# Performance work log

Hardware: AMD Instinct MI355X
Metric: run time of the kernel (lower is better)

The kernel has to match this reference:

```python
import jax, jax.numpy as jnp
import numpy as np

# dims
B, N, FN, FE, H, OUT, MP = 128, 64, 64, 16, 128, 32, 4
P_EDGE = 0.125  # avg degree ~8


def _build_graph_indices():
    """Replicates the torch index construction (nonzero / per-row cat loops)
    with vectorized numpy; done once at setup since adjacency is an input."""
    rng = np.random.default_rng(0)
    up = np.triu(rng.random((B, N, N)) < P_EDGE, 1)
    A = (up | up.transpose(0, 2, 1)).astype(np.int64)  # symmetric, no self-loops
    b_idx, n_idx, nhb_idx = np.nonzero(A)              # row-major, like torch nonzero
    E = b_idx.shape[0]
    ids = np.zeros_like(A)
    ids[b_idx, n_idx, nhb_idx] = np.arange(E) + 1      # adj_of_edge_batch_indices
    deg = A.sum(-1)                                    # [B,N]
    edge_deg = deg[b_idx, nhb_idx]                     # in-degree of each edge's neighbour
    rows = ids[b_idx, nhb_idx, :]                      # [E,N]
    eb = rows[rows > 0] - 1                            # ingoing edge ids, per-row order
    igeb = np.repeat(np.arange(E), edge_deg)           # receiving edge id
    keep = n_idx[igeb] != nhb_idx[eb]                  # drop the reverse edge
    eb, igeb = eb[keep], igeb[keep]
    node_mask = deg != 0                               # [B,N]
    return A, b_idx, n_idx, nhb_idx, eb, igeb, node_mask


def setup_inputs() -> dict:
    key = jax.random.key(0)
    ks = jax.random.split(key, 9)
    A, b_idx, n_idx, nhb_idx, eb, igeb, node_mask = _build_graph_indices()
    s = lambda k, *sh: jax.random.normal(k, sh, jnp.float32) * 0.05
    return {
        "nodes": jax.random.normal(ks[0], (B, N, FN), jnp.float32),
        "edges": jax.random.normal(ks[1], (B, N, N, FE), jnp.float32),
        "W_emb": s(ks[2], FN + FN + FE, H),
        "b_emb": jnp.zeros((H,), jnp.float32),
        "W_msg": s(ks[3], H, H),
        "W_edge": s(ks[4], H, H),
        "b_prop": jnp.zeros((H,), jnp.float32),
        "W_out": s(ks[5], H, OUT),
        "b_out": jnp.zeros((OUT,), jnp.float32),
        "edges_b_idx": jnp.asarray(b_idx),
        "edges_n_idx": jnp.asarray(n_idx),
        "edges_nhb_idx": jnp.asarray(nhb_idx),
        "ing_eb_idx": jnp.asarray(eb),
        "ing_igeb_idx": jnp.asarray(igeb),
        "node_mask": jnp.asarray(node_mask),
    }


def reference(nodes, edges, W_emb, b_emb, W_msg, W_edge, b_prop, W_out, b_out,
              edges_b_idx, edges_n_idx, edges_nhb_idx, ing_eb_idx, ing_igeb_idx,
              node_mask):
    E = edges_b_idx.shape[0]
    Bn, Nn = nodes.shape[0], nodes.shape[1]
    # preprocess_edges: tanh(Linear([node; neighbour; edge]))
    cat = jnp.concatenate([
        nodes[edges_b_idx, edges_n_idx],      # [E,FN]
        nodes[edges_b_idx, edges_nhb_idx],    # [E,FN]
        edges[edges_b_idx, edges_n_idx, edges_nhb_idx],  # [E,FE]
    ], axis=-1)
    e_feat = jnp.tanh(cat @ W_emb + b_emb)    # [E,H]
    # edge-memory message passing; scatter(set)+masked sum == segment_sum over
    # the filtered ingoing-edge pairs (unset slots are zero in the original)
    mem = jnp.zeros((E, W_emb.shape[1]), cat.dtype)
    for _ in range(MP):
        msg = jax.ops.segment_sum(mem[ing_eb_idx], ing_igeb_idx, num_segments=E)
        mem = jnp.tanh(msg @ W_msg + e_feat @ W_edge + b_prop)
    # node_sets scatter + sum over degree slots == segment_sum per receiving node
    node_seg = edges_b_idx * Nn + edges_n_idx
    graph_sets = jax.ops.segment_sum(mem, node_seg, num_segments=Bn * Nn)
    graph_sets = graph_sets.reshape(Bn, Nn, -1)   # [B,N,H]
    # readout: masked sum over nodes, then linear
    g = (graph_sets * node_mask[..., None].astype(cat.dtype)).sum(1)  # [B,H]
    return g @ W_out + b_out
```

## Files before the change

kernel.cpp:

```cpp
#include <hip/hip_runtime.h>
#include <hip/hip_bf16.h>

#define NB 128
#define NN 64
#define HH 128

typedef short bf16x8 __attribute__((ext_vector_type(8)));
typedef float f32x4 __attribute__((ext_vector_type(4)));

static inline int cdiv(int a, int b) { return (a + b - 1) / b; }

__device__ __forceinline__ float tanh_fast(float x) {
    float ax = fabsf(x);
    float ex = __expf(-2.0f * ax);
    float t  = (1.0f - ex) / (1.0f + ex);
    return copysignf(t, x);
}

__device__ __forceinline__ unsigned short f2bfs(float f) {
    unsigned u; __builtin_memcpy(&u, &f, 4);
    u = (u + 0x7FFFu + ((u >> 16) & 1u)) >> 16;
    return (unsigned short)u;
}
__device__ __forceinline__ float bfs2f(unsigned short s) {
    unsigned u = ((unsigned)s) << 16;
    float f; __builtin_memcpy(&f, &u, 4);
    return f;
}
__device__ __forceinline__ int pack2(unsigned short a, unsigned short b) {
    return (int)((unsigned)a | ((unsigned)b << 16));
}
__device__ __forceinline__ f32x4 mfma16(bf16x8 a, bf16x8 b, f32x4 c) {
    return __builtin_amdgcn_mfma_f32_16x16x32_bf16(a, b, c, 0, 0, 0);
}

__global__ void scatter_ids_kernel(const int* __restrict__ bI, const int* __restrict__ nI,
                                   const int* __restrict__ nhI, int* __restrict__ idmat, int E) {
    int e = blockIdx.x * blockDim.x + threadIdx.x;
    if (e >= E) return;
    idmat[((bI[e] << 6) + nI[e]) * NN + nhI[e]] = e;
}
__global__ void build_rev_seg_kernel(const int* __restrict__ bI, const int* __restrict__ nI,
                                     const int* __restrict__ nhI, const int* __restrict__ idmat,
                                     int* __restrict__ rev, int* __restrict__ segnh, int E) {
    int e = blockIdx.x * blockDim.x + threadIdx.x;
    if (e >= E) return;
    int b = bI[e], n = nI[e], nh = nhI[e];
    rev[e]   = idmat[((b << 6) + nh) * NN + n];
    segnh[e] = (b << 6) + nh;
}
__global__ void build_ptr_kernel(const int* __restrict__ bI, const int* __restrict__ nI,
                                 int E, int* __restrict__ ptr) {
    int v = blockIdx.x * blockDim.x + threadIdx.x;
    if (v > NB * NN) return;
    int lo = 0, hi = E;
    while (lo < hi) {
        int mid = (lo + hi) >> 1;
        int sg = (bI[mid] << 6) + nI[mid];
        if (sg < v) lo = mid + 1; else hi = mid;
    }
    ptr[v] = lo;
}
__global__ void prep_w_kernel(const float* __restrict__ W_emb, const float* __restrict__ W_edge,
                              const float* __restrict__ W_msg,
                              unsigned short* __restrict__ WTe, unsigned short* __restrict__ WTd,
                              unsigned short* __restrict__ WTm, float* __restrict__ g) {
    int i = blockIdx.x * blockDim.x + threadIdx.x;
    if (i < 128 * 160) { int c = i / 160, k = i % 160;
        WTe[c * 160 + k] = f2bfs(k < 144 ? W_emb[k * 128 + c] : 0.f); return; }
    i -= 128 * 160;
    if (i < 128 * 128) { int c = i >> 7, k = i & 127;
        WTd[c * 128 + k] = f2bfs(W_edge[k * 128 + c]); return; }
    i -= 128 * 128;
    if (i < 128 * 128) { int c = i >> 7, k = i & 127;
        WTm[c * 128 + k] = f2bfs(W_msg[k * 128 + c]); return; }
    i -= 128 * 128;
    if (i < NB * HH) g[i] = 0.f;
}

__global__ void node_sum_kernel(const unsigned short* __restrict__ mem,
                                const int* __restrict__ ptr, float* __restrict__ S) {
    int v = blockIdx.x, h = threadIdx.x;
    int s = ptr[v], e1 = ptr[v + 1];
    float acc = 0.f;
    for (int e = s; e < e1; ++e) acc += bfs2f(mem[(size_t)e * HH + h]);
    S[(size_t)v * HH + h] = acc;
}

__global__ __launch_bounds__(256) void g01_kernel(
    const float* __restrict__ nodes, const float* __restrict__ edgesF,
    const unsigned short* __restrict__ WTe, const unsigned short* __restrict__ WTd,
    const float* __restrict__ b_emb, const float* __restrict__ b_prop,
    const int* __restrict__ bI, const int* __restrict__ nI, const int* __restrict__ nhI,
    float* __restrict__ ef2, unsigned short* __restrict__ mem1, int E)
{
    __shared__ __align__(16) char lds[51200];
    unsigned short* A = (unsigned short*)lds;
    const int tid = threadIdx.x;
    const int e0  = blockIdx.x * 64;

    for (int s = tid; s < 1280; s += 256) {
        int row = s / 20, kg = s % 20, k0 = kg * 8;
        int e = e0 + row;
        float f0=0,f1=0,f2=0,f3=0,f4=0,f5=0,f6=0,f7=0;
        if (e < E && k0 < 144) {
            int b = bI[e], n = nI[e], nh = nhI[e];
            const float* p;
            if (k0 < 64)        p = nodes  + ((((size_t)b << 6) + n)  << 6) + k0;
            else if (k0 < 128)  p = nodes  + ((((size_t)b << 6) + nh) << 6) + (k0 - 64);
            else                p = edgesF + ((((((size_t)b << 6) + n) << 6) + nh) << 4) + (k0 - 128);
            float4 x = *(const float4*)p, y = *(const float4*)(p + 4);
            f0=x.x; f1=x.y; f2=x.z; f3=x.w; f4=y.x; f5=y.y; f6=y.z; f7=y.w;
        }
        int4 w;
        w.x = pack2(f2bfs(f0), f2bfs(f1)); w.y = pack2(f2bfs(f2), f2bfs(f3));
        w.z = pack2(f2bfs(f4), f2bfs(f5)); w.w = pack2(f2bfs(f6), f2bfs(f7));
        *(int4*)&A[row * 168 + k0] = w;
    }
    __syncthreads();

    const int lane = tid & 63, wid = tid >> 6;
    const int wm = wid & 1, wn = wid >> 1;
    const int l15 = lane & 15, lk = lane >> 4;
    const int r0 = wm * 32, cb = wn * 64;

    f32x4 acc[2][4];
    #pragma unroll
    for (int mi = 0; mi < 2; ++mi)
        #pragma unroll
        for (int ni = 0; ni < 4; ++ni) acc[mi][ni] = (f32x4)0.f;

    #pragma unroll
    for (int ks = 0; ks < 5; ++ks) {
        bf16x8 a0 = *(const bf16x8*)&A[(r0 + l15)      * 168 + ks * 32 + lk * 8];
        bf16x8 a1 = *(const bf16x8*)&A[(r0 + 16 + l15) * 168 + ks * 32 + lk * 8];
        #pragma unroll
        for (int ni = 0; ni < 4; ++ni) {
            bf16x8 bb = *(const bf16x8*)&WTe[(size_t)(cb + ni * 16 + l15) * 160 + ks * 32 + lk * 8];
            acc[0][ni] = mfma16(a0, bb, acc[0][ni]);
            acc[1][ni] = mfma16(a1, bb, acc[1][ni]);
        }
    }
    __syncthreads();

    unsigned short* T = (unsigned short*)lds;
    #pragma unroll
    for (int mi = 0; mi < 2; ++mi)
        #pragma unroll
        for (int ni = 0; ni < 4; ++ni) {
            int col = cb + ni * 16 + l15;
            float be = b_emb[col];
            #pragma unroll
            for (int j = 0; j < 4; ++j) {
                int row = r0 + mi * 16 + lk * 4 + j;
                T[row * 136 + col] = f2bfs(tanh_fast(acc[mi][ni][j] + be));
            }
        }
    __syncthreads();

    f32x4 acc2[2][4];
    #pragma unroll
    for (int mi = 0; mi < 2; ++mi)
        #pragma unroll
        for (int ni = 0; ni < 4; ++ni) acc2[mi][ni] = (f32x4)0.f;

    #pragma unroll
    for (int ks = 0; ks < 4; ++ks) {
        bf16x8 a0 = *(const bf16x8*)&T[(r0 + l15)      * 136 + ks * 32 + lk * 8];
        bf16x8 a1 = *(const bf16x8*)&T[(r0 + 16 + l15) * 136 + ks * 32 + lk * 8];
        #pragma unroll
        for (int ni = 0; ni < 4; ++ni) {
            bf16x8 bb = *(const bf16x8*)&WTd[(size_t)(cb + ni * 16 + l15) * 128 + ks * 32 + lk * 8];
            acc2[0][ni] = mfma16(a0, bb, acc2[0][ni]);
            acc2[1][ni] = mfma16(a1, bb, acc2[1][ni]);
        }
    }
    __syncthreads();

    float*          EF = (float*)lds;
    unsigned short* MB = (unsigned short*)(lds + 64 * 132 * 4);
    #pragma unroll
    for (int mi = 0; mi < 2; ++mi)
        #pragma unroll
        for (int ni = 0; ni < 4; ++ni) {
            int col = cb + ni * 16 + l15;
            float bp = b_prop[col];
            #pragma unroll
            for (int j = 0; j < 4; ++j) {
                int row = r0 + mi * 16 + lk * 4 + j;
                float z = acc2[mi][ni][j] + bp;
                EF[row * 132 + col] = z;
                MB[row * 136 + col] = f2bfs(tanh_fast(z));
            }
        }
    __syncthreads();
    for (int s = tid; s < 2048; s += 256) {
        int row = s >> 5, c0 = (s & 31) * 4, e = e0 + row;
        if (e < E) *(float4*)&ef2[(size_t)e * HH + c0] = *(const float4*)&EF[row * 132 + c0];
    }
    for (int s = tid; s < 1024; s += 256) {
        int row = s >> 4, c0 = (s & 15) * 8, e = e0 + row;
        if (e < E) *(int4*)&mem1[(size_t)e * HH + c0] = *(const int4*)&MB[row * 136 + c0];
    }
}

template <int LAST>
__global__ __launch_bounds__(256) void gmsg_kernel(
    const unsigned short* __restrict__ memIn, const float* __restrict__ S,
    const float* __restrict__ ef2, const unsigned short* __restrict__ WTm,
    const int* __restrict__ rev, const int* __restrict__ segnh,
    unsigned short* __restrict__ memOut, float* __restrict__ g, int E)
{
    __shared__ __align__(16) char lds[17408];
    unsigned short* A = (unsigned short*)lds;
    const int tid = threadIdx.x;
    const int e0  = blockIdx.x * 64;

    for (int s = tid; s < 1024; s += 256) {
        int row = s >> 4, k0 = (s & 15) * 8;
        int e = e0 + row;
        int4 w;
        if (e < E) {
            int sg = segnh[e], rv = rev[e];
            const float* sp = &S[(size_t)sg * HH + k0];
            float4 s0 = *(const float4*)sp, s1 = *(const float4*)(sp + 4);
            int4 mraw = *(const int4*)&memIn[(size_t)rv * HH + k0];
            float m0 = bfs2f((unsigned short)(mraw.x & 0xFFFF)), m1 = bfs2f((unsigned short)((unsigned)mraw.x >> 16));
            float m2 = bfs2f((unsigned short)(mraw.y & 0xFFFF)), m3 = bfs2f((unsigned short)((unsigned)mraw.y >> 16));
            float m4 = bfs2f((unsigned short)(mraw.z & 0xFFFF)), m5 = bfs2f((unsigned short)((unsigned)mraw.z >> 16));
            float m6 = bfs2f((unsigned short)(mraw.w & 0xFFFF)), m7 = bfs2f((unsigned short)((unsigned)mraw.w >> 16));
            w.x = pack2(f2bfs(s0.x - m0), f2bfs(s0.y - m1));
            w.y = pack2(f2bfs(s0.z - m2), f2bfs(s0.w - m3));
            w.z = pack2(f2bfs(s1.x - m4), f2bfs(s1.y - m5));
            w.w = pack2(f2bfs(s1.z - m6), f2bfs(s1.w - m7));
        } else { w.x = w.y = w.z = w.w = 0; }
        *(int4*)&A[row * 136 + k0] = w;
    }
    __syncthreads();

    const int lane = tid & 63, wid = tid >> 6;
    const int wm = wid & 1, wn = wid >> 1;
    const int l15 = lane & 15, lk = lane >> 4;
    const int r0 = wm * 32, cb = wn * 64;

    f32x4 acc[2][4];
    #pragma unroll
    for (int mi = 0; mi < 2; ++mi)
        #pragma unroll
        for (int ni = 0; ni < 4; ++ni) acc[mi][ni] = (f32x4)0.f;

    #pragma unroll
    for (int ks = 0; ks < 4; ++ks) {
        bf16x8 a0 = *(const bf16x8*)&A[(r0 + l15)      * 136 + ks * 32 + lk * 8];
        bf16x8 a1 = *(const bf16x8*)&A[(r0 + 16 + l15) * 136 + ks * 32 + lk * 8];
        #pragma unroll
        for (int ni = 0; ni < 4; ++ni) {
            bf16x8 bb = *(const bf16x8*)&WTm[(size_t)(cb + ni * 16 + l15) * 128 + ks * 32 + lk * 8];
            acc[0][ni] = mfma16(a0, bb, acc[0][ni]);
            acc[1][ni] = mfma16(a1, bb, acc[1][ni]);
        }
    }

    if (LAST) {
        #pragma unroll
        for (int mi = 0; mi < 2; ++mi)
            #pragma unroll
            for (int ni = 0; ni < 4; ++ni) {
                int col = cb + ni * 16 + l15;
                #pragma unroll
                for (int j = 0; j < 4; ++j) {
                    int row = r0 + mi * 16 + lk * 4 + j;
                    int e = e0 + row;
                    if (e < E) {
                        float z = acc[mi][ni][j] + ef2[(size_t)e * HH + col];
                        int b = segnh[e] >> 6;
                        atomicAdd(&g[(size_t)b * HH + col], tanh_fast(z));
                    }
                }
            }
    } else {
        __syncthreads();
        unsigned short* MB = A;
        #pragma unroll
        for (int mi = 0; mi < 2; ++mi)
            #pragma unroll
            for (int ni = 0; ni < 4; ++ni) {
                int col = cb + ni * 16 + l15;
                #pragma unroll
                for (int j = 0; j < 4; ++j) {
                    int row = r0 + mi * 16 + lk * 4 + j;
                    int e = e0 + row;
                    float ez = (e < E) ? ef2[(size_t)e * HH + col] : 0.f;
                    MB[row * 136 + col] = f2bfs(tanh_fast(acc[mi][ni][j] + ez));
                }
            }
        __syncthreads();
        for (int s = tid; s < 1024; s += 256) {
            int row = s >> 4, c0 = (s & 15) * 8, e = e0 + row;
            if (e < E) *(int4*)&memOut[(size_t)e * HH + c0] = *(const int4*)&MB[row * 136 + c0];
        }
    }
}

__global__ void out2_kernel(const float* __restrict__ g, const float* __restrict__ W_out,
                            const float* __restrict__ b_out, float* __restrict__ out) {
    int b = blockIdx.x, tid = threadIdx.x;
    if (tid < 32) {
        float a = b_out[tid];
        for (int h = 0; h < HH; ++h) a += g[(size_t)b * HH + h] * W_out[h * 32 + tid];
        out[b * 32 + tid] = a;
    }
}

extern "C" void kernel_launch(void* const* d_in, const int* in_sizes, int n_in,
                              void* d_out, int out_size, void* d_ws, size_t ws_size,
                              hipStream_t stream) {
    const float* nodes  = (const float*)d_in[0];
    const float* edgesF = (const float*)d_in[1];
    const float* W_emb  = (const float*)d_in[2];
    const float* b_emb  = (const float*)d_in[3];
    const float* W_msg  = (const float*)d_in[4];
    const float* W_edge = (const float*)d_in[5];
    const float* b_prop = (const float*)d_in[6];
    const float* W_out  = (const float*)d_in[7];
    const float* b_out  = (const float*)d_in[8];
    const int*   bI     = (const int*)d_in[9];
    const int*   nI     = (const int*)d_in[10];
    const int*   nhI    = (const int*)d_in[11];
    const int    E      = in_sizes[9];
    float*       out    = (float*)d_out;

    char* ws = (char*)d_ws;
    size_t al = 255;
    size_t szEf  = (((size_t)E * HH * 4) + al) & ~al;
    size_t szMem = (((size_t)E * HH * 2) + al) & ~al;
    size_t szI   = (((size_t)E * 4) + al) & ~al;
    float*          ef2   = (float*)ws;                      ws += szEf;
    unsigned short* memA  = (unsigned short*)ws;             ws += szMem;
    unsigned short* memB  = (unsigned short*)ws;             ws += szMem;
    float*          S     = (float*)ws;                      ws += (size_t)NB * NN * HH * 4;
    float*          g     = (float*)ws;                      ws += (size_t)NB * HH * 4;
    int*            idmat = (int*)ws;                        ws += (size_t)NB * NN * NN * 4;
    int*            rev   = (int*)ws;                        ws += szI;
    int*            segnh = (int*)ws;                        ws += szI;
    int*            ptr   = (int*)ws;                        ws += (((size_t)(NB * NN + 1) * 4) + al) & ~al;
    unsigned short* WTe   = (unsigned short*)ws;             ws += 128 * 160 * 2;
    unsigned short* WTd   = (unsigned short*)ws;             ws += 128 * 128 * 2;
    unsigned short* WTm   = (unsigned short*)ws;             ws += 128 * 128 * 2;

    scatter_ids_kernel  <<<cdiv(E, 256), 256, 0, stream>>>(bI, nI, nhI, idmat, E);
    build_rev_seg_kernel<<<cdiv(E, 256), 256, 0, stream>>>(bI, nI, nhI, idmat, rev, segnh, E);
    build_ptr_kernel    <<<cdiv(NB * NN + 1, 256), 256, 0, stream>>>(bI, nI, E, ptr);
    prep_w_kernel       <<<cdiv(128 * 160 + 2 * 128 * 128 + NB * HH, 256), 256, 0, stream>>>(
                          W_emb, W_edge, W_msg, WTe, WTd, WTm, g);

    const int gb = cdiv(E, 64);
    g01_kernel<<<gb, 256, 0, stream>>>(nodes, edgesF, WTe, WTd, b_emb, b_prop,
                                       bI, nI, nhI, ef2, memA, E);
    node_sum_kernel<<<NB * NN, HH, 0, stream>>>(memA, ptr, S);
    gmsg_kernel<0><<<gb, 256, 0, stream>>>(memA, S, ef2, WTm, rev, segnh, memB, g, E);
    node_sum_kernel<<<NB * NN, HH, 0, stream>>>(memB, ptr, S);
    gmsg_kernel<0><<<gb, 256, 0, stream>>>(memB, S, ef2, WTm, rev, segnh, memA, g, E);
    node_sum_kernel<<<NB * NN, HH, 0, stream>>>(memA, ptr, S);
    gmsg_kernel<1><<<gb, 256, 0, stream>>>(memA, S, ef2, WTm, rev, segnh, nullptr, g, E);

    out2_kernel<<<NB, 64, 0, stream>>>(g, W_out, b_out, out);
}
```

Measured before the change: 342.4 us.

## Fuse node-sum into per-node message-passing kernel with reverse-edge scatter

Replaces the separate node_sum and edge-tiled gmsg kernels with a single per-node kernel. Each one-wave block loads its node's outgoing edge memories into LDS, computes the node sum locally, forms S minus the own-edge term, and multiplies by W_msg with MFMA. It then writes each result to the reverse edge's slot, so the S buffer, segnh array and three launches go away. The cost is tiny 64-thread blocks with 16-row MFMA tiles (low utilisation, padding for low-degree nodes), scattered reverse-edge writes, and per-node atomics in the last step.

```diff
diff --git a/kernel.cpp b/kernel.cpp
--- a/kernel.cpp
+++ b/kernel.cpp
@@ -40,14 +40,12 @@
     if (e >= E) return;
     idmat[((bI[e] << 6) + nI[e]) * NN + nhI[e]] = e;
 }
-__global__ void build_rev_seg_kernel(const int* __restrict__ bI, const int* __restrict__ nI,
-                                     const int* __restrict__ nhI, const int* __restrict__ idmat,
-                                     int* __restrict__ rev, int* __restrict__ segnh, int E) {
+__global__ void build_rev_kernel(const int* __restrict__ bI, const int* __restrict__ nI,
+                                 const int* __restrict__ nhI, const int* __restrict__ idmat,
+                                 int* __restrict__ rev, int E) {
     int e = blockIdx.x * blockDim.x + threadIdx.x;
     if (e >= E) return;
-    int b = bI[e], n = nI[e], nh = nhI[e];
-    rev[e]   = idmat[((b << 6) + nh) * NN + n];
-    segnh[e] = (b << 6) + nh;
+    rev[e] = idmat[((bI[e] << 6) + nhI[e]) * NN + nI[e]];
 }
 __global__ void build_ptr_kernel(const int* __restrict__ bI, const int* __restrict__ nI,
                                  int E, int* __restrict__ ptr) {
@@ -78,15 +76,6 @@
     if (i < NB * HH) g[i] = 0.f;
 }
 
-__global__ void node_sum_kernel(const unsigned short* __restrict__ mem,
-                                const int* __restrict__ ptr, float* __restrict__ S) {
-    int v = blockIdx.x, h = threadIdx.x;
-    int s = ptr[v], e1 = ptr[v + 1];
-    float acc = 0.f;
-    for (int e = s; e < e1; ++e) acc += bfs2f(mem[(size_t)e * HH + h]);
-    S[(size_t)v * HH + h] = acc;
-}
-
 __global__ __launch_bounds__(256) void g01_kernel(
     const float* __restrict__ nodes, const float* __restrict__ edgesF,
     const unsigned short* __restrict__ WTe, const unsigned short* __restrict__ WTd,
@@ -205,100 +194,147 @@
 }
 
 template <int LAST>
-__global__ __launch_bounds__(256) void gmsg_kernel(
-    const unsigned short* __restrict__ memIn, const float* __restrict__ S,
-    const float* __restrict__ ef2, const unsigned short* __restrict__ WTm,
-    const int* __restrict__ rev, const int* __restrict__ segnh,
-    unsigned short* __restrict__ memOut, float* __restrict__ g, int E)
+__global__ __launch_bounds__(64) void mp_kernel(
+    const unsigned short* __restrict__ memIn, const float* __restrict__ ef2,
+    const unsigned short* __restrict__ WTm, const int* __restrict__ rev,
+    const int* __restrict__ ptr, unsigned short* __restrict__ memOut,
+    float* __restrict__ g)
 {
-    __shared__ __align__(16) char lds[17408];
-    unsigned short* A = (unsigned short*)lds;
-    const int tid = threadIdx.x;
-    const int e0  = blockIdx.x * 64;
-
-    for (int s = tid; s < 1024; s += 256) {
-        int row = s >> 4, k0 = (s & 15) * 8;
-        int e = e0 + row;
-        int4 w;
-        if (e < E) {
-            int sg = segnh[e], rv = rev[e];
-            const float* sp = &S[(size_t)sg * HH + k0];
-            float4 s0 = *(const float4*)sp, s1 = *(const float4*)(sp + 4);
-            int4 mraw = *(const int4*)&memIn[(size_t)rv * HH + k0];
-            float m0 = bfs2f((unsigned short)(mraw.x & 0xFFFF)), m1 = bfs2f((unsigned short)((unsigned)mraw.x >> 16));
-            float m2 = bfs2f((unsigned short)(mraw.y & 0xFFFF)), m3 = bfs2f((unsigned short)((unsigned)mraw.y >> 16));
-            float m4 = bfs2f((unsigned short)(mraw.z & 0xFFFF)), m5 = bfs2f((unsigned short)((unsigned)mraw.z >> 16));
-            float m6 = bfs2f((unsigned short)(mraw.w & 0xFFFF)), m7 = bfs2f((unsigned short)((unsigned)mraw.w >> 16));
-            w.x = pack2(f2bfs(s0.x - m0), f2bfs(s0.y - m1));
-            w.y = pack2(f2bfs(s0.z - m2), f2bfs(s0.w - m3));
-            w.z = pack2(f2bfs(s1.x - m4), f2bfs(s1.y - m5));
-            w.w = pack2(f2bfs(s1.z - m6), f2bfs(s1.w - m7));
-        } else { w.x = w.y = w.z = w.w = 0; }
-        *(int4*)&A[row * 136 + k0] = w;
-    }
-    __syncthreads();
-
-    const int lane = tid & 63, wid = tid >> 6;
-    const int wm = wid & 1, wn = wid >> 1;
+    const int u = blockIdx.x;
+    const int s = ptr[u], e1 = ptr[u + 1];
+    const int deg = e1 - s;
+    if (deg == 0) return;
+
+    __shared__ __align__(16) char ldsu[16 * 132 * 4];
+    __shared__ float Srow[128];
+    __shared__ int   rvls[16];
+    unsigned short* A = (unsigned short*)ldsu;
+    float*          C = (float*)ldsu;
+
+    const int lane = threadIdx.x;
     const int l15 = lane & 15, lk = lane >> 4;
-    const int r0 = wm * 32, cb = wn * 64;
-
-    f32x4 acc[2][4];
-    #pragma unroll
-    for (int mi = 0; mi < 2; ++mi)
-        #pragma unroll
-        for (int ni = 0; ni < 4; ++ni) acc[mi][ni] = (f32x4)0.f;
-
-    #pragma unroll
-    for (int ks = 0; ks < 4; ++ks) {
-        bf16x8 a0 = *(const bf16x8*)&A[(r0 + l15)      * 136 + ks * 32 + lk * 8];
-        bf16x8 a1 = *(const bf16x8*)&A[(r0 + 16 + l15) * 136 + ks * 32 + lk * 8];
-        #pragma unroll
-        for (int ni = 0; ni < 4; ++ni) {
-            bf16x8 bb = *(const bf16x8*)&WTm[(size_t)(cb + ni * 16 + l15) * 128 + ks * 32 + lk * 8];
-            acc[0][ni] = mfma16(a0, bb, acc[0][ni]);
-            acc[1][ni] = mfma16(a1, bb, acc[1][ni]);
+
+    {
+        const int m0 = min(deg, 16);
+        #pragma unroll
+        for (int ii = 0; ii < 4; ++ii) {
+            int sl = lane + ii * 64;
+            int r = sl >> 4, k0 = (sl & 15) * 8;
+            int4 w = make_int4(0, 0, 0, 0);
+            if (r < m0) w = *(const int4*)&memIn[(size_t)(s + r) * HH + k0];
+            *(int4*)&A[r * 136 + k0] = w;
+        }
+    }
+    __syncthreads();
+
+    {
+        float s0 = 0.f, s1 = 0.f;
+        const int m0 = min(deg, 16);
+        for (int r = 0; r < m0; ++r) {
+            s0 += bfs2f(A[r * 136 + lane]);
+            s1 += bfs2f(A[r * 136 + lane + 64]);
+        }
+        for (int r = 16; r < deg; ++r) {
+            s0 += bfs2f(memIn[(size_t)(s + r) * HH + lane]);
+            s1 += bfs2f(memIn[(size_t)(s + r) * HH + lane + 64]);
+        }
+        Srow[lane] = s0; Srow[lane + 64] = s1;
+    }
+
+    float ga0 = 0.f, ga1 = 0.f;
+
+    for (int c0 = 0; c0 < deg; c0 += 16) {
+        const int nrows = min(16, deg - c0);
+        if (c0) {
+            __syncthreads();
+            #pragma unroll
+            for (int ii = 0; ii < 4; ++ii) {
+                int sl = lane + ii * 64;
+                int r = sl >> 4, k0 = (sl & 15) * 8;
+                int4 w = make_int4(0, 0, 0, 0);
+                if (r < nrows) w = *(const int4*)&memIn[(size_t)(s + c0 + r) * HH + k0];
+                *(int4*)&A[r * 136 + k0] = w;
+            }
+        }
+        if (lane < nrows) rvls[lane] = rev[s + c0 + lane];
+        __syncthreads();
+
+        #pragma unroll
+        for (int ii = 0; ii < 4; ++ii) {
+            int sl = lane + ii * 64;
+            int r = sl >> 4, k0 = (sl & 15) * 8;
+            int4 w = *(const int4*)&A[r * 136 + k0];
+            unsigned short hs[8];
+            #pragma unroll
+            for (int q = 0; q < 4; ++q) {
+                int raw = (&w.x)[q];
+                float lo = bfs2f((unsigned short)(raw & 0xFFFF));
+                float hi = bfs2f((unsigned short)((unsigned)raw >> 16));
+                hs[2 * q]     = f2bfs(Srow[k0 + 2 * q]     - lo);
+                hs[2 * q + 1] = f2bfs(Srow[k0 + 2 * q + 1] - hi);
+            }
+            int4 o;
+            o.x = pack2(hs[0], hs[1]); o.y = pack2(hs[2], hs[3]);
+            o.z = pack2(hs[4], hs[5]); o.w = pack2(hs[6], hs[7]);
+            *(int4*)&A[r * 136 + k0] = o;
+        }
+        __syncthreads();
+
+        f32x4 acc[8];
+        #pragma unroll
+        for (int ni = 0; ni < 8; ++ni) acc[ni] = (f32x4)0.f;
+        #pragma unroll
+        for (int ks = 0; ks < 4; ++ks) {
+            bf16x8 a = *(const bf16x8*)&A[l15 * 136 + ks * 32 + lk * 8];
+            #pragma unroll
+            for (int ni = 0; ni < 8; ++ni) {
+                bf16x8 bb = *(const bf16x8*)&WTm[(size_t)(ni * 16 + l15) * HH + ks * 32 + lk * 8];
+                acc[ni] = mfma16(a, bb, acc[ni]);
+            }
+        }
+        __syncthreads();
+
+        #pragma unroll
+        for (int ni = 0; ni < 8; ++ni)
+            #pragma unroll
+            for (int j = 0; j < 4; ++j)
+                C[(lk * 4 + j) * 132 + ni * 16 + l15] = acc[ni][j];
+        __syncthreads();
+
+        if (!LAST) {
+            #pragma unroll
+            for (int ii = 0; ii < 4; ++ii) {
+                int sl = lane + ii * 64;
+                int r = sl >> 4, k0 = (sl & 15) * 8;
+                if (r < nrows) {
+                    int rv = rvls[r];
+                    const float* ep = &ef2[(size_t)rv * HH + k0];
+                    float4 f0 = *(const float4*)ep, f1 = *(const float4*)(ep + 4);
+                    const float* cp = &C[r * 132 + k0];
+                    unsigned short hs[8];
+                    hs[0] = f2bfs(tanh_fast(cp[0] + f0.x)); hs[1] = f2bfs(tanh_fast(cp[1] + f0.y));
+                    hs[2] = f2bfs(tanh_fast(cp[2] + f0.z)); hs[3] = f2bfs(tanh_fast(cp[3] + f0.w));
+                    hs[4] = f2bfs(tanh_fast(cp[4] + f1.x)); hs[5] = f2bfs(tanh_fast(cp[5] + f1.y));
+                    hs[6] = f2bfs(tanh_fast(cp[6] + f1.z)); hs[7] = f2bfs(tanh_fast(cp[7] + f1.w));
+                    int4 o;
+                    o.x = pack2(hs[0], hs[1]); o.y = pack2(hs[2], hs[3]);
+                    o.z = pack2(hs[4], hs[5]); o.w = pack2(hs[6], hs[7]);
+                    *(int4*)&memOut[(size_t)rv * HH + k0] = o;
+                }
+            }
+        } else {
+            for (int r = 0; r < nrows; ++r) {
+                int rv = rvls[r];
+                ga0 += tanh_fast(C[r * 132 + lane]      + ef2[(size_t)rv * HH + lane]);
+                ga1 += tanh_fast(C[r * 132 + lane + 64] + ef2[(size_t)rv * HH + lane + 64]);
+            }
         }
     }
 
     if (LAST) {
-        #pragma unroll
-        for (int mi = 0; mi < 2; ++mi)
-            #pragma unroll
-            for (int ni = 0; ni < 4; ++ni) {
-                int col = cb + ni * 16 + l15;
-                #pragma unroll
-                for (int j = 0; j < 4; ++j) {
-                    int row = r0 + mi * 16 + lk * 4 + j;
-                    int e = e0 + row;
-                    if (e < E) {
-                        float z = acc[mi][ni][j] + ef2[(size_t)e * HH + col];
-                        int b = segnh[e] >> 6;
-                        atomicAdd(&g[(size_t)b * HH + col], tanh_fast(z));
-                    }
-                }
-            }
-    } else {
-        __syncthreads();
-        unsigned short* MB = A;
-        #pragma unroll
-        for (int mi = 0; mi < 2; ++mi)
-            #pragma unroll
-            for (int ni = 0; ni < 4; ++ni) {
-                int col = cb + ni * 16 + l15;
-                #pragma unroll
-                for (int j = 0; j < 4; ++j) {
-                    int row = r0 + mi * 16 + lk * 4 + j;
-                    int e = e0 + row;
-                    float ez = (e < E) ? ef2[(size_t)e * HH + col] : 0.f;
-                    MB[row * 136 + col] = f2bfs(tanh_fast(acc[mi][ni][j] + ez));
-                }
-            }
-        __syncthreads();
-        for (int s = tid; s < 1024; s += 256) {
-            int row = s >> 4, c0 = (s & 15) * 8, e = e0 + row;
-            if (e < E) *(int4*)&memOut[(size_t)e * HH + c0] = *(const int4*)&MB[row * 136 + c0];
-        }
+        const int b = u >> 6;
+        atomicAdd(&g[(size_t)b * HH + lane],      ga0);
+        atomicAdd(&g[(size_t)b * HH + lane + 64], ga1);
     }
 }
 
@@ -338,31 +374,26 @@
     float*          ef2   = (float*)ws;                      ws += szEf;
     unsigned short* memA  = (unsigned short*)ws;             ws += szMem;
     unsigned short* memB  = (unsigned short*)ws;             ws += szMem;
-    float*          S     = (float*)ws;                      ws += (size_t)NB * NN * HH * 4;
     float*          g     = (float*)ws;                      ws += (size_t)NB * HH * 4;
     int*            idmat = (int*)ws;                        ws += (size_t)NB * NN * NN * 4;
     int*            rev   = (int*)ws;                        ws += szI;
-    int*            segnh = (int*)ws;                        ws += szI;
     int*            ptr   = (int*)ws;                        ws += (((size_t)(NB * NN + 1) * 4) + al) & ~al;
     unsigned short* WTe   = (unsigned short*)ws;             ws += 128 * 160 * 2;
     unsigned short* WTd   = (unsigned short*)ws;             ws += 128 * 128 * 2;
     unsigned short* WTm   = (unsigned short*)ws;             ws += 128 * 128 * 2;
 
-    scatter_ids_kernel  <<<cdiv(E, 256), 256, 0, stream>>>(bI, nI, nhI, idmat, E);
-    build_rev_seg_kernel<<<cdiv(E, 256), 256, 0, stream>>>(bI, nI, nhI, idmat, rev, segnh, E);
-    build_ptr_kernel    <<<cdiv(NB * NN + 1, 256), 256, 0, stream>>>(bI, nI, E, ptr);
-    prep_w_kernel       <<<cdiv(128 * 160 + 2 * 128 * 128 + NB * HH, 256), 256, 0, stream>>>(
-                          W_emb, W_edge, W_msg, WTe, WTd, WTm, g);
+    scatter_ids_kernel<<<cdiv(E, 256), 256, 0, stream>>>(bI, nI, nhI, idmat, E);
+    build_rev_kernel  <<<cdiv(E, 256), 256, 0, stream>>>(bI, nI, nhI, idmat, rev, E);
+    build_ptr_kernel  <<<cdiv(NB * NN + 1, 256), 256, 0, stream>>>(bI, nI, E, ptr);
+    prep_w_kernel     <<<cdiv(128 * 160 + 2 * 128 * 128 + NB * HH, 256), 256, 0, stream>>>(
+                        W_emb, W_edge, W_msg, WTe, WTd, WTm, g);
 
     const int gb = cdiv(E, 64);
     g01_kernel<<<gb, 256, 0, stream>>>(nodes, edgesF, WTe, WTd, b_emb, b_prop,
                                        bI, nI, nhI, ef2, memA, E);
-    node_sum_kernel<<<NB * NN, HH, 0, stream>>>(memA, ptr, S);
-    gmsg_kernel<0><<<gb, 256, 0, stream>>>(memA, S, ef2, WTm, rev, segnh, memB, g, E);
-    node_sum_kernel<<<NB * NN, HH, 0, stream>>>(memB, ptr, S);
-    gmsg_kernel<0><<<gb, 256, 0, stream>>>(memB, S, ef2, WTm, rev, segnh, memA, g, E);
-    node_sum_kernel<<<NB * NN, HH, 0, stream>>>(memA, ptr, S);
-    gmsg_kernel<1><<<gb, 256, 0, stream>>>(memA, S, ef2, WTm, rev, segnh, nullptr, g, E);
+    mp_kernel<0><<<NB * NN, 64, 0, stream>>>(memA, ef2, WTm, rev, ptr, memB, nullptr);
+    mp_kernel<0><<<NB * NN, 64, 0, stream>>>(memB, ef2, WTm, rev, ptr, memA, nullptr);
+    mp_kernel<1><<<NB * NN, 64, 0, stream>>>(memA, ef2, WTm, rev, ptr, nullptr, g);
 
     out2_kernel<<<NB, 64, 0, stream>>>(g, W_out, b_out, out);
 }
```

Result: faster. 286.9 us (-16.2%).
